# Kernel tuning notes

Hardware: AMD Instinct MI355X
Metric: run time of the kernel (lower is better)

Reference implementation:

```python
import jax, jax.numpy as jnp
import numpy as np

# Irreps structure: (multiplicity, component dim 2l+1) for 64x0e + 32x1o + 16x2e
MULTS = (64, 32, 16)
DIMS = (1, 3, 5)
N_NODES = 65536
NUM_TYPES = 64


def setup_inputs() -> dict:
    key = jax.random.key(0)
    k_x, k_idx, k0, k1, k2 = jax.random.split(key, 5)
    dim = sum(m * d for m, d in zip(MULTS, DIMS))  # 240
    x = jax.random.normal(k_x, (N_NODES, dim), dtype=jnp.float32)
    idx = jax.random.randint(k_idx, (N_NODES,), 0, NUM_TYPES)
    W0 = jax.random.normal(k0, (NUM_TYPES, 64, 64), dtype=jnp.float32)
    W1 = jax.random.normal(k1, (NUM_TYPES, 32, 32), dtype=jnp.float32)
    W2 = jax.random.normal(k2, (NUM_TYPES, 16, 16), dtype=jnp.float32)
    return {"x": x, "W0": W0, "W1": W1, "W2": W2, "idx": idx}


def reference(x, W0, W1, W2, idx):
    """Indexed e3nn-style linear: per-node index gathers a weight set; each
    irrep block mixes multiplicity channels (shared across the 2l+1 components)
    with e3nn path normalization 1/sqrt(m_in)."""
    n = x.shape[0]
    outs = []
    off = 0
    for W, m, d in zip((W0, W1, W2), MULTS, DIMS):
        blk = x[:, off:off + m * d].reshape(n, m, d)  # [N, m_in, 2l+1]
        off += m * d
        Wn = W[idx]  # gather per-node weights: [N, m_in, m_out]
        scale = np.float32(1.0 / np.sqrt(m))
        out = jnp.einsum('nio,nid->nod', Wn, blk) * scale  # [N, m_out, 2l+1]
        outs.append(out.reshape(n, m * d))
    return jnp.concatenate(outs, axis=-1)
```

## Files before the change

kernel.cpp:

```cpp
#include <hip/hip_runtime.h>

typedef __attribute__((ext_vector_type(8))) short short8;
typedef __attribute__((ext_vector_type(4))) float floatx4;

#define NTYPES 64
#define BPT 16
#define NB  64

#define WS_HIST   0
#define WS_SCAN   4096
#define WS_CNT    8192
#define WS_OFF    8256
#define WS_LIST   8320

#define WT0_OFF 0
#define WT1_OFF 4608
#define WT2_OFF 5888
#define SMEM_USH 6528

__device__ __forceinline__ unsigned short f2bf(float f) {
    union { float f; unsigned u; } v; v.f = f;
    unsigned u = v.u;
    u += 0x7FFFu + ((u >> 16) & 1u);
    return (unsigned short)(u >> 16);
}

__global__ __launch_bounds__(256) void hist_kernel(const int* __restrict__ idx,
                                                   int* __restrict__ ws, int n) {
    __shared__ int h[NTYPES];
    const int b = blockIdx.x, tid = threadIdx.x;
    if (tid < NTYPES) h[tid] = 0;
    __syncthreads();
    const int seg = (n + NB - 1) / NB;
    const int lo = b * seg, hi = min(lo + seg, n);
    for (int e = lo + tid; e < hi; e += 256) atomicAdd(&h[idx[e]], 1);
    __syncthreads();
    if (tid < NTYPES) ws[WS_HIST + tid * NB + b] = h[tid];
}

__global__ __launch_bounds__(256) void scan_kernel(int* __restrict__ ws, int n) {
    __shared__ int partial[256];
    const int tid = threadIdx.x;
    int v[16];
    int s = 0;
    const int base = tid * 16;
#pragma unroll
    for (int k = 0; k < 16; ++k) { v[k] = ws[WS_HIST + base + k]; s += v[k]; }
    partial[tid] = s;
    __syncthreads();
    for (int d = 1; d < 256; d <<= 1) {
        int t = (tid >= d) ? partial[tid - d] : 0;
        __syncthreads();
        partial[tid] += t;
        __syncthreads();
    }
    int excl = (tid == 0) ? 0 : partial[tid - 1];
#pragma unroll
    for (int k = 0; k < 16; ++k) { ws[WS_SCAN + base + k] = excl; excl += v[k]; }
    __syncthreads();
    if (tid < NTYPES) {
        int start = ws[WS_SCAN + tid * NB];
        int end   = (tid == NTYPES - 1) ? partial[255] : ws[WS_SCAN + (tid + 1) * NB];
        ws[WS_OFF + tid] = start;
        ws[WS_CNT + tid] = end - start;
    }
}

__global__ __launch_bounds__(256) void scatter_kernel(const int* __restrict__ idx,
                                                      int* __restrict__ ws, int n) {
    __shared__ int cur[NTYPES];
    const int b = blockIdx.x, tid = threadIdx.x;
    if (tid < NTYPES) cur[tid] = ws[WS_SCAN + tid * NB + b];
    __syncthreads();
    const int seg = (n + NB - 1) / NB;
    const int lo = b * seg, hi = min(lo + seg, n);
    for (int e = lo + tid; e < hi; e += 256) {
        int pos = atomicAdd(&cur[idx[e]], 1);
        ws[WS_LIST + pos] = e;
    }
}

__device__ __forceinline__ short8 pack8(const float* xv) {
    short8 a;
#pragma unroll
    for (int j = 0; j < 8; ++j) a[j] = (short)f2bf(xv[j]);
    return a;
}

__global__ __launch_bounds__(256) void main_kernel(
    const float* __restrict__ x,
    const float* __restrict__ W0,
    const float* __restrict__ W1,
    const float* __restrict__ W2,
    const int* __restrict__ ws,
    float* __restrict__ out)
{
    __shared__ __align__(16) unsigned short sm[SMEM_USH];

    const int ty  = blockIdx.y;
    const int tid = threadIdx.x;

    {
        const float* w = W0 + (size_t)ty * 64 * 64;
        for (int e = tid; e < 4096; e += 256) {
            int i = e >> 6, o = e & 63;
            sm[WT0_OFF + o * 72 + i] = f2bf(w[e] * 0.125f);
        }
        const float* w1 = W1 + (size_t)ty * 32 * 32;
        for (int e = tid; e < 1024; e += 256) {
            int i = e >> 5, o = e & 31;
            sm[WT1_OFF + o * 40 + i] = f2bf(w1[e] * 0.17677669529663687f);
        }
        const float* w2 = W2 + (size_t)ty * 16 * 16;
        {
            int e = tid & 255;
            int i = e >> 4, o = e & 15;
            sm[WT2_OFF + o * 40 + i]      = f2bf(w2[e] * 0.25f);
            sm[WT2_OFF + o * 40 + 16 + i] = 0;
        }
    }
    __syncthreads();

    const int cnt = ws[WS_CNT + ty];
    const int off = ws[WS_OFF + ty];
    const int* list = ws + WS_LIST;

    const int wv = tid >> 6, ln = tid & 63;
    const int r = ln & 15, q4 = ln >> 4;
    const int slot = blockIdx.x * 4 + wv;

    for (int base = slot * 16; base < cnt; base += BPT * 4 * 16) {
        int gi = min(base + r, cnt - 1);
        int nd = list[off + gi];
        const size_t xb = (size_t)nd * 240;

        int nr[4]; bool vst[4];
#pragma unroll
        for (int rr = 0; rr < 4; ++rr) {
            int row = q4 * 4 + rr;
            nr[rr]  = __shfl(nd, row);
            vst[rr] = (base + row) < cnt;
        }

        {
            float4 f0 = *(const float4*)(x + xb + q4 * 8);
            float4 f1 = *(const float4*)(x + xb + q4 * 8 + 4);
            float4 f2 = *(const float4*)(x + xb + 32 + q4 * 8);
            float4 f3 = *(const float4*)(x + xb + 32 + q4 * 8 + 4);
            float v0[8] = {f0.x, f0.y, f0.z, f0.w, f1.x, f1.y, f1.z, f1.w};
            float v1[8] = {f2.x, f2.y, f2.z, f2.w, f3.x, f3.y, f3.z, f3.w};
            short8 a0 = pack8(v0), a1 = pack8(v1);
#pragma unroll
            for (int nt = 0; nt < 4; ++nt) {
                short8 b0 = *(const short8*)(sm + WT0_OFF + (nt * 16 + r) * 72 + q4 * 8);
                short8 b1 = *(const short8*)(sm + WT0_OFF + (nt * 16 + r) * 72 + 32 + q4 * 8);
                floatx4 acc = {0.f, 0.f, 0.f, 0.f};
                acc = __builtin_amdgcn_mfma_f32_16x16x32_bf16(a0, b0, acc, 0, 0, 0);
                acc = __builtin_amdgcn_mfma_f32_16x16x32_bf16(a1, b1, acc, 0, 0, 0);
#pragma unroll
                for (int rr = 0; rr < 4; ++rr)
                    if (vst[rr]) out[(size_t)nr[rr] * 240 + nt * 16 + r] = acc[rr];
            }
        }

        {
            short8 b0 = *(const short8*)(sm + WT1_OFF + r * 40 + q4 * 8);
            short8 b1 = *(const short8*)(sm + WT1_OFF + (16 + r) * 40 + q4 * 8);
#pragma unroll
            for (int d = 0; d < 3; ++d) {
                float xv[8];
#pragma unroll
                for (int j = 0; j < 8; ++j)
                    xv[j] = x[xb + 64 + (size_t)(q4 * 8 + j) * 3 + d];
                short8 a = pack8(xv);
                floatx4 acc = {0.f, 0.f, 0.f, 0.f};
                acc = __builtin_amdgcn_mfma_f32_16x16x32_bf16(a, b0, acc, 0, 0, 0);
#pragma unroll
                for (int rr = 0; rr < 4; ++rr)
                    if (vst[rr]) out[(size_t)nr[rr] * 240 + 64 + r * 3 + d] = acc[rr];
                floatx4 acc2 = {0.f, 0.f, 0.f, 0.f};
                acc2 = __builtin_amdgcn_mfma_f32_16x16x32_bf16(a, b1, acc2, 0, 0, 0);
#pragma unroll
                for (int rr = 0; rr < 4; ++rr)
                    if (vst[rr]) out[(size_t)nr[rr] * 240 + 64 + (16 + r) * 3 + d] = acc2[rr];
            }
        }

        {
            short8 b = *(const short8*)(sm + WT2_OFF + r * 40 + q4 * 8);
#pragma unroll
            for (int d = 0; d < 5; ++d) {
                short8 a = {0, 0, 0, 0, 0, 0, 0, 0};
                if (q4 < 2) {
                    float xv[8];
#pragma unroll
                    for (int j = 0; j < 8; ++j)
                        xv[j] = x[xb + 160 + (size_t)(q4 * 8 + j) * 5 + d];
                    a = pack8(xv);
                }
                floatx4 acc = {0.f, 0.f, 0.f, 0.f};
                acc = __builtin_amdgcn_mfma_f32_16x16x32_bf16(a, b, acc, 0, 0, 0);
#pragma unroll
                for (int rr = 0; rr < 4; ++rr)
                    if (vst[rr]) out[(size_t)nr[rr] * 240 + 160 + r * 5 + d] = acc[rr];
            }
        }
    }
}

extern "C" void kernel_launch(void* const* d_in, const int* in_sizes, int n_in,
                              void* d_out, int out_size, void* d_ws, size_t ws_size,
                              hipStream_t stream) {
    const float* x  = (const float*)d_in[0];
    const float* W0 = (const float*)d_in[1];
    const float* W1 = (const float*)d_in[2];
    const float* W2 = (const float*)d_in[3];
    const int*   idx = (const int*)d_in[4];
    float* out = (float*)d_out;
    const int n = in_sizes[4];
    int* ws = (int*)d_ws;

    hist_kernel   <<<NB, 256, 0, stream>>>(idx, ws, n);
    scan_kernel   <<<1, 256, 0, stream>>>(ws, n);
    scatter_kernel<<<NB, 256, 0, stream>>>(idx, ws, n);
    main_kernel   <<<dim3(BPT, NTYPES), 256, 0, stream>>>(x, W0, W1, W2, ws, out);
}
```

Baseline: 163.1 us.

## Stage x rows and outputs through per-wave LDS for coalesced float4 traffic

Each wave now loads its 16 gathered node rows of x with coalesced float4 reads, converts them to bf16 into a per-wave LDS tile, and builds the MFMA operands from LDS instead of issuing strided scalar global loads for the l=1 and l=2 blocks. Results are also staged in LDS and written back as float4 stores per row instead of scattered scalar stores. This targets uncoalesced global access at the cost of extra LDS space (about 38 KB per block) and LDS bank traffic. The launch bounds also gain an occupancy hint of 3 blocks.

```diff
diff --git a/kernel.cpp b/kernel.cpp
--- a/kernel.cpp
+++ b/kernel.cpp
@@ -16,7 +16,9 @@
 #define WT0_OFF 0
 #define WT1_OFF 4608
 #define WT2_OFF 5888
-#define SMEM_USH 6528
+#define WT_END  6528
+#define XS_USH  3968
+#define SMEM_USH (WT_END + 4 * XS_USH)
 
 __device__ __forceinline__ unsigned short f2bf(float f) {
     union { float f; unsigned u; } v; v.f = f;
@@ -80,14 +82,7 @@
     }
 }
 
-__device__ __forceinline__ short8 pack8(const float* xv) {
-    short8 a;
-#pragma unroll
-    for (int j = 0; j < 8; ++j) a[j] = (short)f2bf(xv[j]);
-    return a;
-}
-
-__global__ __launch_bounds__(256) void main_kernel(
+__global__ __launch_bounds__(256, 3) void main_kernel(
     const float* __restrict__ x,
     const float* __restrict__ W0,
     const float* __restrict__ W1,
@@ -96,6 +91,7 @@
     float* __restrict__ out)
 {
     __shared__ __align__(16) unsigned short sm[SMEM_USH];
+    float* smf = (float*)sm;
 
     const int ty  = blockIdx.y;
     const int tid = threadIdx.x;
@@ -127,82 +123,116 @@
 
     const int wv = tid >> 6, ln = tid & 63;
     const int r = ln & 15, q4 = ln >> 4;
+    const int XS = WT_END + wv * XS_USH;
+    const int FB = XS >> 1;
     const int slot = blockIdx.x * 4 + wv;
 
     for (int base = slot * 16; base < cnt; base += BPT * 4 * 16) {
         int gi = min(base + r, cnt - 1);
         int nd = list[off + gi];
-        const size_t xb = (size_t)nd * 240;
-
-        int nr[4]; bool vst[4];
-#pragma unroll
-        for (int rr = 0; rr < 4; ++rr) {
-            int row = q4 * 4 + rr;
-            nr[rr]  = __shfl(nd, row);
-            vst[rr] = (base + row) < cnt;
-        }
-
-        {
-            float4 f0 = *(const float4*)(x + xb + q4 * 8);
-            float4 f1 = *(const float4*)(x + xb + q4 * 8 + 4);
-            float4 f2 = *(const float4*)(x + xb + 32 + q4 * 8);
-            float4 f3 = *(const float4*)(x + xb + 32 + q4 * 8 + 4);
-            float v0[8] = {f0.x, f0.y, f0.z, f0.w, f1.x, f1.y, f1.z, f1.w};
-            float v1[8] = {f2.x, f2.y, f2.z, f2.w, f3.x, f3.y, f3.z, f3.w};
-            short8 a0 = pack8(v0), a1 = pack8(v1);
+
+#pragma unroll
+        for (int t = 0; t < 15; ++t) {
+            int idx = t * 64 + ln;
+            int row = idx / 60, c4 = idx - row * 60;
+            int nod = __shfl(nd, row);
+            float4 f = *(const float4*)(x + (size_t)nod * 240 + c4 * 4);
+            ushort4 u;
+            u.x = f2bf(f.x); u.y = f2bf(f.y); u.z = f2bf(f.z); u.w = f2bf(f.w);
+            *(ushort4*)(sm + XS + row * 248 + c4 * 4) = u;
+        }
+
+        short8 a00 = *(const short8*)(sm + XS + r * 248 + q4 * 8);
+        short8 a01 = *(const short8*)(sm + XS + r * 248 + 32 + q4 * 8);
+        short8 a1[3];
+#pragma unroll
+        for (int d = 0; d < 3; ++d)
+#pragma unroll
+            for (int j = 0; j < 8; ++j)
+                ((unsigned short*)&a1[d])[j] = sm[XS + r * 248 + 64 + (q4 * 8 + j) * 3 + d];
+        short8 a2[5];
+#pragma unroll
+        for (int d = 0; d < 5; ++d) {
+            a2[d] = short8{0, 0, 0, 0, 0, 0, 0, 0};
+            if (q4 < 2)
+#pragma unroll
+                for (int j = 0; j < 8; ++j)
+                    ((unsigned short*)&a2[d])[j] = sm[XS + r * 248 + 160 + (q4 * 8 + j) * 5 + d];
+        }
+
+        {
+            floatx4 acc[4];
 #pragma unroll
             for (int nt = 0; nt < 4; ++nt) {
                 short8 b0 = *(const short8*)(sm + WT0_OFF + (nt * 16 + r) * 72 + q4 * 8);
                 short8 b1 = *(const short8*)(sm + WT0_OFF + (nt * 16 + r) * 72 + 32 + q4 * 8);
-                floatx4 acc = {0.f, 0.f, 0.f, 0.f};
-                acc = __builtin_amdgcn_mfma_f32_16x16x32_bf16(a0, b0, acc, 0, 0, 0);
-                acc = __builtin_amdgcn_mfma_f32_16x16x32_bf16(a1, b1, acc, 0, 0, 0);
+                acc[nt] = floatx4{0.f, 0.f, 0.f, 0.f};
+                acc[nt] = __builtin_amdgcn_mfma_f32_16x16x32_bf16(a00, b0, acc[nt], 0, 0, 0);
+                acc[nt] = __builtin_amdgcn_mfma_f32_16x16x32_bf16(a01, b1, acc[nt], 0, 0, 0);
+            }
+#pragma unroll
+            for (int nt = 0; nt < 4; ++nt)
 #pragma unroll
                 for (int rr = 0; rr < 4; ++rr)
-                    if (vst[rr]) out[(size_t)nr[rr] * 240 + nt * 16 + r] = acc[rr];
+                    smf[FB + (q4 * 4 + rr) * 68 + nt * 16 + r] = acc[nt][rr];
+#pragma unroll
+            for (int t = 0; t < 4; ++t) {
+                int idx = t * 64 + ln;
+                int row = idx >> 4, c4 = idx & 15;
+                float4 v = *(const float4*)(smf + FB + row * 68 + c4 * 4);
+                int nod = __shfl(nd, row);
+                if (base + row < cnt) *(float4*)(out + (size_t)nod * 240 + c4 * 4) = v;
             }
         }
 
         {
             short8 b0 = *(const short8*)(sm + WT1_OFF + r * 40 + q4 * 8);
             short8 b1 = *(const short8*)(sm + WT1_OFF + (16 + r) * 40 + q4 * 8);
+            floatx4 acc[6];
 #pragma unroll
             for (int d = 0; d < 3; ++d) {
-                float xv[8];
-#pragma unroll
-                for (int j = 0; j < 8; ++j)
-                    xv[j] = x[xb + 64 + (size_t)(q4 * 8 + j) * 3 + d];
-                short8 a = pack8(xv);
-                floatx4 acc = {0.f, 0.f, 0.f, 0.f};
-                acc = __builtin_amdgcn_mfma_f32_16x16x32_bf16(a, b0, acc, 0, 0, 0);
+                acc[d * 2]     = floatx4{0.f, 0.f, 0.f, 0.f};
+                acc[d * 2]     = __builtin_amdgcn_mfma_f32_16x16x32_bf16(a1[d], b0, acc[d * 2], 0, 0, 0);
+                acc[d * 2 + 1] = floatx4{0.f, 0.f, 0.f, 0.f};
+                acc[d * 2 + 1] = __builtin_amdgcn_mfma_f32_16x16x32_bf16(a1[d], b1, acc[d * 2 + 1], 0, 0, 0);
+            }
+#pragma unroll
+            for (int d = 0; d < 3; ++d)
+#pragma unroll
+                for (int h = 0; h < 2; ++h)
+#pragma unroll
+                    for (int rr = 0; rr < 4; ++rr)
+                        smf[FB + (q4 * 4 + rr) * 100 + (h * 16 + r) * 3 + d] = acc[d * 2 + h][rr];
+#pragma unroll
+            for (int t = 0; t < 6; ++t) {
+                int idx = t * 64 + ln;
+                int row = idx / 24, c4 = idx - row * 24;
+                float4 v = *(const float4*)(smf + FB + row * 100 + c4 * 4);
+                int nod = __shfl(nd, row);
+                if (base + row < cnt) *(float4*)(out + (size_t)nod * 240 + 64 + c4 * 4) = v;
+            }
+        }
+
+        {
+            short8 b = *(const short8*)(sm + WT2_OFF + r * 40 + q4 * 8);
+            floatx4 acc[5];
+#pragma unroll
+            for (int d = 0; d < 5; ++d) {
+                acc[d] = floatx4{0.f, 0.f, 0.f, 0.f};
+                acc[d] = __builtin_amdgcn_mfma_f32_16x16x32_bf16(a2[d], b, acc[d], 0, 0, 0);
+            }
+#pragma unroll
+            for (int d = 0; d < 5; ++d)
 #pragma unroll
                 for (int rr = 0; rr < 4; ++rr)
-                    if (vst[rr]) out[(size_t)nr[rr] * 240 + 64 + r * 3 + d] = acc[rr];
-                floatx4 acc2 = {0.f, 0.f, 0.f, 0.f};
-                acc2 = __builtin_amdgcn_mfma_f32_16x16x32_bf16(a, b1, acc2, 0, 0, 0);
-#pragma unroll
-                for (int rr = 0; rr < 4; ++rr)
-                    if (vst[rr]) out[(size_t)nr[rr] * 240 + 64 + (16 + r) * 3 + d] = acc2[rr];
-            }
-        }
-
-        {
-            short8 b = *(const short8*)(sm + WT2_OFF + r * 40 + q4 * 8);
-#pragma unroll
-            for (int d = 0; d < 5; ++d) {
-                short8 a = {0, 0, 0, 0, 0, 0, 0, 0};
-                if (q4 < 2) {
-                    float xv[8];
-#pragma unroll
-                    for (int j = 0; j < 8; ++j)
-                        xv[j] = x[xb + 160 + (size_t)(q4 * 8 + j) * 5 + d];
-                    a = pack8(xv);
-                }
-                floatx4 acc = {0.f, 0.f, 0.f, 0.f};
-                acc = __builtin_amdgcn_mfma_f32_16x16x32_bf16(a, b, acc, 0, 0, 0);
-#pragma unroll
-                for (int rr = 0; rr < 4; ++rr)
-                    if (vst[rr]) out[(size_t)nr[rr] * 240 + 160 + r * 5 + d] = acc[rr];
+                    smf[FB + (q4 * 4 + rr) * 84 + r * 5 + d] = acc[d][rr];
+#pragma unroll
+            for (int t = 0; t < 5; ++t) {
+                int idx = t * 64 + ln;
+                int row = idx / 20, c4 = idx - row * 20;
+                float4 v = *(const float4*)(smf + FB + row * 84 + c4 * 4);
+                int nod = __shfl(nd, row);
+                if (base + row < cnt) *(float4*)(out + (size_t)nod * 240 + 160 + c4 * 4) = v;
             }
         }
     }
```

After: 179.7 us. 10.2% more time.

## Replace global type sort with per-block local bucketing and pre-packed bf16 weights

Applied to the files above, without the earlier changes.

Drops the global histogram/scan/scatter pipeline. Each 512-thread block now loads 256 contiguous node rows into shared memory as bf16 with coalesced reads, buckets those rows by type locally into 16-row tiles, and runs MFMA per tile using weights pre-transposed into an MFMA-friendly bf16 layout by a small prepass kernel. This removes two launches and the scattered x gathers. In exchange it adds partially filled tiles for each type in every block, serial tile building on thread 0, and weight reads from global/L2 instead of LDS. It also uses a large shared buffer and allows only one block per CU.

```diff
diff --git a/kernel.cpp b/kernel.cpp
--- a/kernel.cpp
+++ b/kernel.cpp
@@ -3,20 +3,12 @@
 typedef __attribute__((ext_vector_type(8))) short short8;
 typedef __attribute__((ext_vector_type(4))) float floatx4;
 
-#define NTYPES 64
-#define BPT 16
-#define NB  64
-
-#define WS_HIST   0
-#define WS_SCAN   4096
-#define WS_CNT    8192
-#define WS_OFF    8256
-#define WS_LIST   8320
-
-#define WT0_OFF 0
-#define WT1_OFF 4608
-#define WT2_OFF 5888
-#define SMEM_USH 6528
+#define NTYPES   64
+#define ROWS_PB  256
+#define THREADS  512
+#define NW       8
+#define MAXTILES 80
+#define WT_STRIDE 5632
 
 __device__ __forceinline__ unsigned short f2bf(float f) {
     union { float f; unsigned u; } v; v.f = f;
@@ -25,184 +17,159 @@
     return (unsigned short)(u >> 16);
 }
 
-__global__ __launch_bounds__(256) void hist_kernel(const int* __restrict__ idx,
-                                                   int* __restrict__ ws, int n) {
-    __shared__ int h[NTYPES];
-    const int b = blockIdx.x, tid = threadIdx.x;
-    if (tid < NTYPES) h[tid] = 0;
-    __syncthreads();
-    const int seg = (n + NB - 1) / NB;
-    const int lo = b * seg, hi = min(lo + seg, n);
-    for (int e = lo + tid; e < hi; e += 256) atomicAdd(&h[idx[e]], 1);
-    __syncthreads();
-    if (tid < NTYPES) ws[WS_HIST + tid * NB + b] = h[tid];
-}
-
-__global__ __launch_bounds__(256) void scan_kernel(int* __restrict__ ws, int n) {
-    __shared__ int partial[256];
-    const int tid = threadIdx.x;
-    int v[16];
-    int s = 0;
-    const int base = tid * 16;
-#pragma unroll
-    for (int k = 0; k < 16; ++k) { v[k] = ws[WS_HIST + base + k]; s += v[k]; }
-    partial[tid] = s;
-    __syncthreads();
-    for (int d = 1; d < 256; d <<= 1) {
-        int t = (tid >= d) ? partial[tid - d] : 0;
-        __syncthreads();
-        partial[tid] += t;
-        __syncthreads();
+__global__ __launch_bounds__(256) void wt_kernel(const float* __restrict__ W0,
+                                                 const float* __restrict__ W1,
+                                                 const float* __restrict__ W2,
+                                                 unsigned short* __restrict__ wt) {
+    const int t = blockIdx.x, tid = threadIdx.x;
+    unsigned short* dst = wt + (size_t)t * WT_STRIDE;
+    const float* w0 = W0 + (size_t)t * 4096;
+    for (int e = tid; e < 4096; e += 256) {
+        int f = e >> 9, rem = e & 511, rr = rem >> 5, k2 = rem & 31;
+        int i = (f & 1) * 32 + k2, o = (f >> 1) * 16 + rr;
+        dst[e] = f2bf(w0[i * 64 + o] * 0.125f);
     }
-    int excl = (tid == 0) ? 0 : partial[tid - 1];
-#pragma unroll
-    for (int k = 0; k < 16; ++k) { ws[WS_SCAN + base + k] = excl; excl += v[k]; }
-    __syncthreads();
-    if (tid < NTYPES) {
-        int start = ws[WS_SCAN + tid * NB];
-        int end   = (tid == NTYPES - 1) ? partial[255] : ws[WS_SCAN + (tid + 1) * NB];
-        ws[WS_OFF + tid] = start;
-        ws[WS_CNT + tid] = end - start;
+    const float* w1 = W1 + (size_t)t * 1024;
+    for (int e = tid; e < 1024; e += 256) {
+        int h = e >> 9, rem = e & 511, rr = rem >> 5, k = rem & 31;
+        dst[4096 + e] = f2bf(w1[k * 32 + h * 16 + rr] * 0.17677669529663687f);
+    }
+    const float* w2 = W2 + (size_t)t * 256;
+    for (int e = tid; e < 512; e += 256) {
+        int rr = e >> 5, k = e & 31;
+        dst[5120 + e] = (k < 16) ? f2bf(w2[k * 16 + rr] * 0.25f) : (unsigned short)0;
     }
 }
 
-__global__ __launch_bounds__(256) void scatter_kernel(const int* __restrict__ idx,
-                                                      int* __restrict__ ws, int n) {
-    __shared__ int cur[NTYPES];
+__global__ __launch_bounds__(THREADS, 1) void main_kernel(
+    const float* __restrict__ x,
+    const int* __restrict__ gidx,
+    const unsigned short* __restrict__ wt,
+    float* __restrict__ out, int n)
+{
+    __shared__ __align__(16) unsigned short xrow[ROWS_PB * 240];
+    __shared__ int cnts[NTYPES], cur[NTYPES];
+    __shared__ unsigned short tlist[ROWS_PB];
+    __shared__ unsigned short ttype[MAXTILES], tstt[MAXTILES], trws[MAXTILES];
+    __shared__ int ntiles;
+
     const int b = blockIdx.x, tid = threadIdx.x;
-    if (tid < NTYPES) cur[tid] = ws[WS_SCAN + tid * NB + b];
-    __syncthreads();
-    const int seg = (n + NB - 1) / NB;
-    const int lo = b * seg, hi = min(lo + seg, n);
-    for (int e = lo + tid; e < hi; e += 256) {
-        int pos = atomicAdd(&cur[idx[e]], 1);
-        ws[WS_LIST + pos] = e;
-    }
-}
+    const int nbase = b * ROWS_PB;
+    const int nvalid = min(ROWS_PB, n - nbase);
 
-__device__ __forceinline__ short8 pack8(const float* xv) {
-    short8 a;
 #pragma unroll
-    for (int j = 0; j < 8; ++j) a[j] = (short)f2bf(xv[j]);
-    return a;
-}
-
-__global__ __launch_bounds__(256) void main_kernel(
-    const float* __restrict__ x,
-    const float* __restrict__ W0,
-    const float* __restrict__ W1,
-    const float* __restrict__ W2,
-    const int* __restrict__ ws,
-    float* __restrict__ out)
-{
-    __shared__ __align__(16) unsigned short sm[SMEM_USH];
-
-    const int ty  = blockIdx.y;
-    const int tid = threadIdx.x;
-
-    {
-        const float* w = W0 + (size_t)ty * 64 * 64;
-        for (int e = tid; e < 4096; e += 256) {
-            int i = e >> 6, o = e & 63;
-            sm[WT0_OFF + o * 72 + i] = f2bf(w[e] * 0.125f);
-        }
-        const float* w1 = W1 + (size_t)ty * 32 * 32;
-        for (int e = tid; e < 1024; e += 256) {
-            int i = e >> 5, o = e & 31;
-            sm[WT1_OFF + o * 40 + i] = f2bf(w1[e] * 0.17677669529663687f);
-        }
-        const float* w2 = W2 + (size_t)ty * 16 * 16;
-        {
-            int e = tid & 255;
-            int i = e >> 4, o = e & 15;
-            sm[WT2_OFF + o * 40 + i]      = f2bf(w2[e] * 0.25f);
-            sm[WT2_OFF + o * 40 + 16 + i] = 0;
+    for (int t = 0; t < 30; ++t) {
+        int e = t * THREADS + tid;
+        int row = e / 60, c4 = e - row * 60;
+        if (row < nvalid) {
+            float4 f = *(const float4*)(x + (size_t)(nbase + row) * 240 + c4 * 4);
+            ushort4 u;
+            u.x = f2bf(f.x); u.y = f2bf(f.y); u.z = f2bf(f.z); u.w = f2bf(f.w);
+            *(ushort4*)(xrow + row * 240 + c4 * 4) = u;
         }
     }
+
+    if (tid < NTYPES) cnts[tid] = 0;
     __syncthreads();
-
-    const int cnt = ws[WS_CNT + ty];
-    const int off = ws[WS_OFF + ty];
-    const int* list = ws + WS_LIST;
+    int myty = -1;
+    if (tid < nvalid) { myty = gidx[nbase + tid]; atomicAdd(&cnts[myty], 1); }
+    __syncthreads();
+    if (tid == 0) {
+        int acc = 0, ntl = 0;
+        for (int t = 0; t < NTYPES; ++t) {
+            int c = cnts[t];
+            cur[t] = acc;
+            for (int s = 0; s < c; s += 16) {
+                ttype[ntl] = (unsigned short)t;
+                tstt[ntl]  = (unsigned short)(acc + s);
+                trws[ntl]  = (unsigned short)min(16, c - s);
+                ++ntl;
+            }
+            acc += c;
+        }
+        ntiles = ntl;
+    }
+    __syncthreads();
+    if (tid < nvalid) { int p = atomicAdd(&cur[myty], 1); tlist[p] = (unsigned short)tid; }
+    __syncthreads();
 
     const int wv = tid >> 6, ln = tid & 63;
     const int r = ln & 15, q4 = ln >> 4;
-    const int slot = blockIdx.x * 4 + wv;
+    const int NT = ntiles;
 
-    for (int base = slot * 16; base < cnt; base += BPT * 4 * 16) {
-        int gi = min(base + r, cnt - 1);
-        int nd = list[off + gi];
-        const size_t xb = (size_t)nd * 240;
+    for (int ti = wv; ti < NT; ti += NW) {
+        const int ty = ttype[ti], st = tstt[ti], rows = trws[ti];
+        const int lr = tlist[st + min(r, rows - 1)];
+        const unsigned short* xr = xrow + lr * 240;
 
-        int nr[4]; bool vst[4];
+        short8 a00 = *(const short8*)(xr + q4 * 8);
+        short8 a01 = *(const short8*)(xr + 32 + q4 * 8);
+        short8 a1[3];
+#pragma unroll
+        for (int d = 0; d < 3; ++d)
+#pragma unroll
+            for (int j = 0; j < 8; ++j)
+                ((unsigned short*)&a1[d])[j] = xr[64 + (q4 * 8 + j) * 3 + d];
+        short8 a2[5];
+#pragma unroll
+        for (int d = 0; d < 5; ++d) {
+            a2[d] = short8{0, 0, 0, 0, 0, 0, 0, 0};
+            if (q4 < 2)
+#pragma unroll
+                for (int j = 0; j < 8; ++j)
+                    ((unsigned short*)&a2[d])[j] = xr[160 + (q4 * 8 + j) * 5 + d];
+        }
+
+        size_t ob[4]; bool vr[4];
 #pragma unroll
         for (int rr = 0; rr < 4; ++rr) {
-            int row = q4 * 4 + rr;
-            nr[rr]  = __shfl(nd, row);
-            vst[rr] = (base + row) < cnt;
+            int rowi = q4 * 4 + rr;
+            vr[rr] = rowi < rows;
+            int lrr = __shfl(lr, rowi);
+            ob[rr] = (size_t)(nbase + lrr) * 240;
+        }
+
+        const unsigned short* wb = wt + (size_t)ty * WT_STRIDE;
+
+#pragma unroll
+        for (int nt = 0; nt < 4; ++nt) {
+            short8 b0 = *(const short8*)(wb + (nt * 2) * 512 + r * 32 + q4 * 8);
+            short8 b1 = *(const short8*)(wb + (nt * 2 + 1) * 512 + r * 32 + q4 * 8);
+            floatx4 ac = {0.f, 0.f, 0.f, 0.f};
+            ac = __builtin_amdgcn_mfma_f32_16x16x32_bf16(a00, b0, ac, 0, 0, 0);
+            ac = __builtin_amdgcn_mfma_f32_16x16x32_bf16(a01, b1, ac, 0, 0, 0);
+#pragma unroll
+            for (int rr = 0; rr < 4; ++rr)
+                if (vr[rr]) out[ob[rr] + nt * 16 + r] = ac[rr];
         }
 
         {
-            float4 f0 = *(const float4*)(x + xb + q4 * 8);
-            float4 f1 = *(const float4*)(x + xb + q4 * 8 + 4);
-            float4 f2 = *(const float4*)(x + xb + 32 + q4 * 8);
-            float4 f3 = *(const float4*)(x + xb + 32 + q4 * 8 + 4);
-            float v0[8] = {f0.x, f0.y, f0.z, f0.w, f1.x, f1.y, f1.z, f1.w};
-            float v1[8] = {f2.x, f2.y, f2.z, f2.w, f3.x, f3.y, f3.z, f3.w};
-            short8 a0 = pack8(v0), a1 = pack8(v1);
+            short8 c0 = *(const short8*)(wb + 4096 + r * 32 + q4 * 8);
+            short8 c1 = *(const short8*)(wb + 4096 + 512 + r * 32 + q4 * 8);
 #pragma unroll
-            for (int nt = 0; nt < 4; ++nt) {
-                short8 b0 = *(const short8*)(sm + WT0_OFF + (nt * 16 + r) * 72 + q4 * 8);
-                short8 b1 = *(const short8*)(sm + WT0_OFF + (nt * 16 + r) * 72 + 32 + q4 * 8);
-                floatx4 acc = {0.f, 0.f, 0.f, 0.f};
-                acc = __builtin_amdgcn_mfma_f32_16x16x32_bf16(a0, b0, acc, 0, 0, 0);
-                acc = __builtin_amdgcn_mfma_f32_16x16x32_bf16(a1, b1, acc, 0, 0, 0);
+            for (int d = 0; d < 3; ++d) {
+                floatx4 ac = {0.f, 0.f, 0.f, 0.f};
+                ac = __builtin_amdgcn_mfma_f32_16x16x32_bf16(a1[d], c0, ac, 0, 0, 0);
 #pragma unroll
                 for (int rr = 0; rr < 4; ++rr)
-                    if (vst[rr]) out[(size_t)nr[rr] * 240 + nt * 16 + r] = acc[rr];
+                    if (vr[rr]) out[ob[rr] + 64 + r * 3 + d] = ac[rr];
+                floatx4 ac2 = {0.f, 0.f, 0.f, 0.f};
+                ac2 = __builtin_amdgcn_mfma_f32_16x16x32_bf16(a1[d], c1, ac2, 0, 0, 0);
+#pragma unroll
+                for (int rr = 0; rr < 4; ++rr)
+                    if (vr[rr]) out[ob[rr] + 64 + (16 + r) * 3 + d] = ac2[rr];
             }
         }
 
         {
-            short8 b0 = *(const short8*)(sm + WT1_OFF + r * 40 + q4 * 8);
-            short8 b1 = *(const short8*)(sm + WT1_OFF + (16 + r) * 40 + q4 * 8);
+            short8 c2 = *(const short8*)(wb + 5120 + r * 32 + q4 * 8);
 #pragma unroll
-            for (int d = 0; d < 3; ++d) {
-                float xv[8];
-#pragma unroll
-                for (int j = 0; j < 8; ++j)
-                    xv[j] = x[xb + 64 + (size_t)(q4 * 8 + j) * 3 + d];
-                short8 a = pack8(xv);
-                floatx4 acc = {0.f, 0.f, 0.f, 0.f};
-                acc = __builtin_amdgcn_mfma_f32_16x16x32_bf16(a, b0, acc, 0, 0, 0);
+            for (int d = 0; d < 5; ++d) {
+                floatx4 ac = {0.f, 0.f, 0.f, 0.f};
+                ac = __builtin_amdgcn_mfma_f32_16x16x32_bf16(a2[d], c2, ac, 0, 0, 0);
 #pragma unroll
                 for (int rr = 0; rr < 4; ++rr)
-                    if (vst[rr]) out[(size_t)nr[rr] * 240 + 64 + r * 3 + d] = acc[rr];
-                floatx4 acc2 = {0.f, 0.f, 0.f, 0.f};
-                acc2 = __builtin_amdgcn_mfma_f32_16x16x32_bf16(a, b1, acc2, 0, 0, 0);
-#pragma unroll
-                for (int rr = 0; rr < 4; ++rr)
-                    if (vst[rr]) out[(size_t)nr[rr] * 240 + 64 + (16 + r) * 3 + d] = acc2[rr];
-            }
-        }
-
-        {
-            short8 b = *(const short8*)(sm + WT2_OFF + r * 40 + q4 * 8);
-#pragma unroll
-            for (int d = 0; d < 5; ++d) {
-                short8 a = {0, 0, 0, 0, 0, 0, 0, 0};
-                if (q4 < 2) {
-                    float xv[8];
-#pragma unroll
-                    for (int j = 0; j < 8; ++j)
-                        xv[j] = x[xb + 160 + (size_t)(q4 * 8 + j) * 5 + d];
-                    a = pack8(xv);
-                }
-                floatx4 acc = {0.f, 0.f, 0.f, 0.f};
-                acc = __builtin_amdgcn_mfma_f32_16x16x32_bf16(a, b, acc, 0, 0, 0);
-#pragma unroll
-                for (int rr = 0; rr < 4; ++rr)
-                    if (vst[rr]) out[(size_t)nr[rr] * 240 + 160 + r * 5 + d] = acc[rr];
+                    if (vr[rr]) out[ob[rr] + 160 + r * 5 + d] = ac[rr];
             }
         }
     }
@@ -218,10 +185,8 @@
     const int*   idx = (const int*)d_in[4];
     float* out = (float*)d_out;
     const int n = in_sizes[4];
-    int* ws = (int*)d_ws;
+    unsigned short* wt = (unsigned short*)d_ws;
 
-    hist_kernel   <<<NB, 256, 0, stream>>>(idx, ws, n);
-    scan_kernel   <<<1, 256, 0, stream>>>(ws, n);
-    scatter_kernel<<<NB, 256, 0, stream>>>(idx, ws, n);
-    main_kernel   <<<dim3(BPT, NTYPES), 256, 0, stream>>>(x, W0, W1, W2, ws, out);
+    wt_kernel  <<<NTYPES, 256, 0, stream>>>(W0, W1, W2, wt);
+    main_kernel<<<(n + ROWS_PB - 1) / ROWS_PB, THREADS, 0, stream>>>(x, idx, wt, out, n);
 }
```

New measurement: 160.9 us. About the same (-1.4%).
